# Optimization experiments

Measured on AMD Instinct MI355X. Metric: run time of the kernel, lower is better.

The kernel has to match this reference:

```python
import jax, jax.numpy as jnp
import numpy as np

D_MODEL = 1024
N_HEADS = 16
D_K = D_MODEL // N_HEADS
B, T = 4, 2048


def setup_inputs() -> dict:
    key = jax.random.key(0)
    ks = jax.random.split(key, 13)
    s = 1.0 / np.sqrt(D_MODEL)
    inp = {
        "Q": jax.random.normal(ks[0], (B, T, D_MODEL), jnp.float32),
        "K": jax.random.normal(ks[1], (B, T, D_MODEL), jnp.float32),
        "V": jax.random.normal(ks[2], (B, T, D_MODEL), jnp.float32),
        "mask": jax.random.randint(ks[3], (B, 1, 1, T), 0, 2, jnp.int32),
        "W_q": jax.random.normal(ks[4], (D_MODEL, D_MODEL), jnp.float32) * s,
        "b_q": jax.random.normal(ks[5], (D_MODEL,), jnp.float32) * s,
        "W_k": jax.random.normal(ks[6], (D_MODEL, D_MODEL), jnp.float32) * s,
        "b_k": jax.random.normal(ks[7], (D_MODEL,), jnp.float32) * s,
        "W_v": jax.random.normal(ks[8], (D_MODEL, D_MODEL), jnp.float32) * s,
        "b_v": jax.random.normal(ks[9], (D_MODEL,), jnp.float32) * s,
        "W_o": jax.random.normal(ks[10], (D_MODEL, D_MODEL), jnp.float32) * s,
        "b_o": jax.random.normal(ks[11], (D_MODEL,), jnp.float32) * s,
    }
    return inp


def _split_heads(x):
    # (B, T, d_model) -> (B, H, T, d_k)
    b, t, _ = x.shape
    return x.reshape(b, t, N_HEADS, D_K).transpose(0, 2, 1, 3)


def reference(Q, K, V, mask, W_q, b_q, W_k, b_k, W_v, b_v, W_o, b_o):
    # Linear projections (torch nn.Linear: x @ W.T + b)
    q = _split_heads(Q @ W_q.T + b_q)  # (B, H, T, d_k)
    k = _split_heads(K @ W_k.T + b_k)
    v = _split_heads(V @ W_v.T + b_v)

    scale = 1.0 / jnp.sqrt(jnp.asarray(D_K, q.dtype))
    scores = jnp.einsum('bhqd,bhkd->bhqk', q, k) * scale  # (B, H, T, T)
    scores = jnp.where(mask == 0, -jnp.inf, scores)
    attn = jax.nn.softmax(scores, axis=-1)
    out = jnp.einsum('bhqk,bhkd->bhqd', attn, v)  # (B, H, T, d_k)

    # combine heads: (B, H, T, d_k) -> (B, T, d_model)
    bsz, h, t, dk = out.shape
    out = out.transpose(0, 2, 1, 3).reshape(bsz, t, h * dk)
    return out @ W_o.T + b_o
```

## Files before the change

### kernel.cpp

```cpp
#include <hip/hip_runtime.h>
#include <hip/hip_bf16.h>
#include <stdint.h>

#define NHEADS 16
#define SEQ    2048
#define DMODEL 1024
#define DK     64

#define QB_OFF  0ull
#define KB_OFF  8388608ull
#define VB_OFF  16777216ull
#define WQ_OFF  25165824ull
#define WK_OFF  26214400ull
#define WV_OFF  27262976ull
#define WO_OFF  28311552ull
#define QH_OFF  29360128ull
#define KH_OFF  37748736ull
#define VT_OFF  46137344ull
#define MSKF_OFF 54525952ull
#define OC_OFF  0ull

typedef __attribute__((ext_vector_type(8))) __bf16 bf16x8;
typedef __attribute__((ext_vector_type(4))) float  floatx4;

__device__ __forceinline__ unsigned short f2bf(float f) {
  unsigned int u = __float_as_uint(f);
  u += 0x7fffu + ((u >> 16) & 1u);
  return (unsigned short)(u >> 16);
}

__device__ __forceinline__ void gld_lds16(const void* g, void* l) {
  __builtin_amdgcn_global_load_lds(
      (const __attribute__((address_space(1))) unsigned int*)(g),
      (__attribute__((address_space(3))) unsigned int*)(uintptr_t)(l),
      16, 0, 0);
}

struct CastArgs {
  const float* src[8];
  unsigned long long off[8];
  unsigned int n[8];
};

__global__ __launch_bounds__(256) void cast_bf16(CastArgs a, unsigned short* __restrict__ ws) {
  int ti = blockIdx.y;
  unsigned int n = a.n[ti];
  unsigned int stride = gridDim.x * blockDim.x * 4u;
  unsigned int i0 = (blockIdx.x * blockDim.x + threadIdx.x) * 4u;
  if (ti == 7) {
    const int* s = (const int*)a.src[7];
    unsigned short* d = ws + a.off[7];
    for (unsigned int i = i0; i < n; i += stride) {
      int4 v = *(const int4*)(s + i);
      ushort4 o;
      o.x = v.x ? 0x3f80u : 0u;
      o.y = v.y ? 0x3f80u : 0u;
      o.z = v.z ? 0x3f80u : 0u;
      o.w = v.w ? 0x3f80u : 0u;
      unsigned int p = (i & ~31u) | ((i & 12u) << 1) | ((i & 16u) >> 2) | (i & 3u);
      *(ushort4*)(d + p) = o;
    }
    return;
  }
  const float* s = a.src[ti];
  unsigned short* d = ws + a.off[ti];
  for (unsigned int i = i0; i < n; i += stride) {
    float4 v = *(const float4*)(s + i);
    ushort4 o;
    o.x = f2bf(v.x); o.y = f2bf(v.y); o.z = f2bf(v.z); o.w = f2bf(v.w);
    *(ushort4*)(d + i) = o;
  }
}

__device__ __forceinline__ void gemm_core_128(
    const unsigned short* __restrict__ A, const unsigned short* __restrict__ Bw,
    int m0, int n0, unsigned short* As, unsigned short* Bs, floatx4 acc[4][4])
{
  int tid = threadIdx.x;
  int lane = tid & 63, l16 = lane & 15, quad = lane >> 4;
  int wave = tid >> 6, wm = wave >> 1, wn = wave & 1;
  #pragma unroll 1
  for (int kt = 0; kt < 32; ++kt) {
    __syncthreads();
    #pragma unroll
    for (int rnd = 0; rnd < 2; ++rnd) {
      int e = tid * 8 + rnd * 2048;
      int row = e >> 5, col = e & 31;
      gld_lds16(A  + (size_t)(m0 + row) * 1024 + kt * 32 + col, As + e);
      gld_lds16(Bw + (size_t)(n0 + row) * 1024 + kt * 32 + col, Bs + e);
    }
    __syncthreads();
    bf16x8 af[4], bfr[4];
    #pragma unroll
    for (int f = 0; f < 4; ++f) {
      af[f]  = *(const bf16x8*)(As + (wm * 64 + f * 16 + l16) * 32 + quad * 8);
      bfr[f] = *(const bf16x8*)(Bs + (wn * 64 + f * 16 + l16) * 32 + quad * 8);
    }
    #pragma unroll
    for (int fm = 0; fm < 4; ++fm)
      #pragma unroll
      for (int fn = 0; fn < 4; ++fn)
        acc[fm][fn] = __builtin_amdgcn_mfma_f32_16x16x32_bf16(af[fm], bfr[fn], acc[fm][fn], 0, 0, 0);
  }
}

__global__ __launch_bounds__(256) void proj_gemm(
    const unsigned short* __restrict__ wsc, unsigned short* __restrict__ ws,
    const float* __restrict__ bq, const float* __restrict__ bk, const float* __restrict__ bv)
{
  __shared__ unsigned short smem[17408];
  unsigned short* As = smem;
  unsigned short* Bs = smem + 4096;
  int z = blockIdx.z;
  int tid = threadIdx.x, lane = tid & 63, l16 = lane & 15, quad = lane >> 4;
  int wave = tid >> 6, wm = wave >> 1, wn = wave & 1;

  if (z < 2) {
    const unsigned short* A  = wsc + (z == 0 ? QB_OFF : KB_OFF);
    const unsigned short* Bw = wsc + (z == 0 ? WQ_OFF : WK_OFF);
    const float* bias = (z == 0) ? bq : bk;
    unsigned short* dst = ws + (z == 0 ? QH_OFF : KH_OFF);
    float scale = (z == 0) ? 0.18033688011111772f : 1.0f;

    int flat = blockIdx.y * 8 + blockIdx.x;
    int xcd = flat & 7, slot = flat >> 3;
    int m_t = xcd * 8 + (slot >> 3);
    int n_t = slot & 7;
    int m0 = m_t * 128, n0 = n_t * 128;
    floatx4 acc[4][4] = {};
    gemm_core_128(A, Bw, m0, n0, As, Bs, acc);

    __syncthreads();
    #pragma unroll
    for (int fn = 0; fn < 4; ++fn) {
      int c = wn * 64 + fn * 16 + l16;
      float bvv = bias[n0 + c];
      #pragma unroll
      for (int fm = 0; fm < 4; ++fm)
        #pragma unroll
        for (int r = 0; r < 4; ++r) {
          int t = wm * 64 + fm * 16 + quad * 4 + r;
          smem[t * 136 + c] = f2bf((acc[fm][fn][r] + bvv) * scale);
        }
    }
    __syncthreads();
    #pragma unroll
    for (int it = 0; it < 8; ++it) {
      int e = it * 2048 + tid * 8;
      int t = e >> 7, c = e & 127;
      uint4 val = *(const uint4*)(smem + t * 136 + c);
      int m = m0 + t, b = m >> 11, tg = m & 2047;
      int h = (n0 + c) >> 6, d = (n0 + c) & 63;
      *(uint4*)(dst + ((size_t)(b * NHEADS + h) * SEQ + tg) * DK + d) = val;
    }
  } else {
    int flat = blockIdx.y * 8 + blockIdx.x;
    int b = flat >> 7, rem = flat & 127;
    int mt = rem >> 4, nt = rem & 15;
    int m0 = mt * 128, n0 = nt * 128;
    const unsigned short* A  = wsc + WV_OFF;
    const unsigned short* Bw = wsc + VB_OFF + (size_t)b * SEQ * DMODEL;
    unsigned short* dst = ws + VT_OFF;

    floatx4 acc[4][4] = {};
    gemm_core_128(A, Bw, m0, n0, As, Bs, acc);

    const unsigned short* pm = wsc + MSKF_OFF + (size_t)b * SEQ;
    int tpl[4];
    float mv[4];
    #pragma unroll
    for (int fn = 0; fn < 4; ++fn) {
      int t = wn * 64 + fn * 16 + l16;
      int tp = (t & ~31) | ((t & 12) << 1) | ((t & 16) >> 2) | (t & 3);
      tpl[fn] = tp;
      mv[fn] = __uint_as_float((unsigned int)pm[n0 + tp] << 16);
    }

    __syncthreads();
    #pragma unroll
    for (int fm = 0; fm < 4; ++fm) {
      int mb = m0 + wm * 64 + fm * 16 + quad * 4;
      float4 bb4 = *(const float4*)(bv + mb);
      float bbv[4] = {bb4.x, bb4.y, bb4.z, bb4.w};
      #pragma unroll
      for (int r = 0; r < 4; ++r) {
        int mrow = wm * 64 + fm * 16 + quad * 4 + r;
        #pragma unroll
        for (int fn = 0; fn < 4; ++fn)
          smem[mrow * 136 + tpl[fn]] = f2bf((acc[fm][fn][r] + bbv[r]) * mv[fn]);
      }
    }
    __syncthreads();
    #pragma unroll
    for (int it = 0; it < 8; ++it) {
      int e = it * 2048 + tid * 8;
      int mrow = e >> 7, tcol = e & 127;
      uint4 val = *(const uint4*)(smem + mrow * 136 + tcol);
      int m = m0 + mrow, h = m >> 6, d = m & 63;
      *(uint4*)(dst + ((size_t)(b * NHEADS + h) * DK + d) * SEQ + n0 + tcol) = val;
    }
  }
}

__global__ __launch_bounds__(128, 2) void attn_fused(
    const unsigned short* __restrict__ wsc, unsigned short* __restrict__ ws)
{
  __shared__ unsigned short smem[16640];
  unsigned short* Ks  = smem;
  unsigned short* Vts = smem + 8192;
  unsigned short* MskB = smem + 16384;

  int fid = blockIdx.y * gridDim.x + blockIdx.x;
  int xcd = fid & 7, slot = fid >> 3;
  int bh = xcd * 8 + (slot >> 4);
  int qt = slot & 15;
  int b = bh >> 4, h = bh & 15;
  int tid = threadIdx.x, wave = tid >> 6, lane = tid & 63, l16 = lane & 15, quad = lane >> 4;
  int wq = wave * 64;

  const unsigned short* qh = wsc + QH_OFF + (size_t)bh * SEQ * DK;
  const unsigned short* kh = wsc + KH_OFF + (size_t)bh * SEQ * DK;
  const unsigned short* vt = wsc + VT_OFF + (size_t)bh * DK * SEQ;
  const unsigned short* pm = wsc + MSKF_OFF + (size_t)b * SEQ;

  #pragma unroll
  for (int kk = 0; kk < 2; ++kk)
    #pragma unroll
    for (int rnd = 0; rnd < 4; ++rnd) {
      int e = tid * 8 + rnd * 1024;
      int row = e >> 5, col = e & 31;
      gld_lds16(qh + (size_t)(qt * 128 + row) * DK + kk * 32 + col, Ks + kk * 4096 + e);
    }
  __syncthreads();
  bf16x8 qf[4][2];
  #pragma unroll
  for (int fq = 0; fq < 4; ++fq)
    #pragma unroll
    for (int kk = 0; kk < 2; ++kk)
      qf[fq][kk] = *(const bf16x8*)(Ks + kk * 4096 + (wq + fq * 16 + l16) * 32 + quad * 8);
  __syncthreads();

  #pragma unroll
  for (int kk = 0; kk < 2; ++kk)
    #pragma unroll
    for (int rnd = 0; rnd < 4; ++rnd) {
      int e = tid * 8 + rnd * 1024;
      int row = e >> 5, col = e & 31;
      gld_lds16(kh + (size_t)row * DK + kk * 32 + col, Ks + kk * 4096 + e);
    }
  if (tid < 16)
    gld_lds16(pm + tid * 8, MskB + tid * 8);
  __syncthreads();

  floatx4 o[4][4] = {};
  floatx4 osum[4] = {};
  const floatx4 zero4 = {};

  union PU { unsigned int u[4][4]; bf16x8 v[4]; };

  #pragma unroll 1
  for (int jt = 0; jt < 16; ++jt) {
    #pragma unroll
    for (int kk = 0; kk < 4; ++kk)
      #pragma unroll
      for (int rnd = 0; rnd < 2; ++rnd) {
        int e = tid * 8 + rnd * 1024;
        int row = e >> 5, col = e & 31;
        gld_lds16(vt + (size_t)row * SEQ + jt * 128 + kk * 32 + col, Vts + kk * 2048 + e);
      }

    PU pf[4];
    #pragma unroll
    for (int w = 0; w < 4; ++w) {
      floatx4 s[2][4];
      #pragma unroll
      for (int f2 = 0; f2 < 2; ++f2) {
        int fk = 2 * w + f2;
        bf16x8 kf0 = *(const bf16x8*)(Ks +        (fk * 16 + l16) * 32 + quad * 8);
        bf16x8 kf1 = *(const bf16x8*)(Ks + 4096 + (fk * 16 + l16) * 32 + quad * 8);
        #pragma unroll
        for (int fq = 0; fq < 4; ++fq) {
          s[f2][fq] = __builtin_amdgcn_mfma_f32_16x16x32_bf16(kf0, qf[fq][0], zero4, 0, 0, 0);
          s[f2][fq] = __builtin_amdgcn_mfma_f32_16x16x32_bf16(kf1, qf[fq][1], s[f2][fq], 0, 0, 0);
        }
      }
      #pragma unroll
      for (int f2 = 0; f2 < 2; ++f2)
        #pragma unroll
        for (int fq = 0; fq < 4; ++fq)
          #pragma unroll
          for (int r = 0; r < 4; ++r)
            s[f2][fq][r] = __builtin_amdgcn_exp2f(s[f2][fq][r]);

      #pragma unroll
      for (int fq = 0; fq < 4; ++fq) {
        asm("v_cvt_pk_bf16_f32 %0, %1, %2" : "=v"(pf[w].u[fq][0]) : "v"(s[0][fq][0]), "v"(s[0][fq][1]));
        asm("v_cvt_pk_bf16_f32 %0, %1, %2" : "=v"(pf[w].u[fq][1]) : "v"(s[0][fq][2]), "v"(s[0][fq][3]));
        asm("v_cvt_pk_bf16_f32 %0, %1, %2" : "=v"(pf[w].u[fq][2]) : "v"(s[1][fq][0]), "v"(s[1][fq][1]));
        asm("v_cvt_pk_bf16_f32 %0, %1, %2" : "=v"(pf[w].u[fq][3]) : "v"(s[1][fq][2]), "v"(s[1][fq][3]));
      }

      bf16x8 mvf = *(const bf16x8*)(MskB + w * 32 + quad * 8);
      #pragma unroll
      for (int fq = 0; fq < 4; ++fq)
        osum[fq] = __builtin_amdgcn_mfma_f32_16x16x32_bf16(mvf, pf[w].v[fq], osum[fq], 0, 0, 0);
    }

    __syncthreads();

    if (jt < 15) {
      const unsigned short* khn = kh + (size_t)(jt + 1) * 128 * DK;
      #pragma unroll
      for (int kk = 0; kk < 2; ++kk)
        #pragma unroll
        for (int rnd = 0; rnd < 4; ++rnd) {
          int e = tid * 8 + rnd * 1024;
          int row = e >> 5, col = e & 31;
          gld_lds16(khn + (size_t)row * DK + kk * 32 + col, Ks + kk * 4096 + e);
        }
      if (tid < 16)
        gld_lds16(pm + (jt + 1) * 128 + tid * 8, MskB + tid * 8);
    }

    __builtin_amdgcn_s_setprio(1);
    #pragma unroll
    for (int w = 0; w < 4; ++w)
      #pragma unroll
      for (int fd = 0; fd < 4; ++fd) {
        bf16x8 vf = *(const bf16x8*)(Vts + w * 2048 + (fd * 16 + l16) * 32 + quad * 8);
        #pragma unroll
        for (int fq = 0; fq < 4; ++fq)
          o[fd][fq] = __builtin_amdgcn_mfma_f32_16x16x32_bf16(vf, pf[w].v[fq], o[fd][fq], 0, 0, 0);
      }
    __builtin_amdgcn_s_setprio(0);

    __syncthreads();
  }

  float inv[4];
  #pragma unroll
  for (int fq = 0; fq < 4; ++fq)
    inv[fq] = __builtin_amdgcn_rcpf(osum[fq][0]);

  unsigned short* Ot = smem;
  #pragma unroll
  for (int fd = 0; fd < 4; ++fd)
    #pragma unroll
    for (int fq = 0; fq < 4; ++fq)
      #pragma unroll
      for (int r = 0; r < 4; ++r) {
        int q = wq + fq * 16 + l16;
        int d = fd * 16 + quad * 4 + r;
        Ot[q * 72 + d] = f2bf(o[fd][fq][r] * inv[fq]);
      }
  __syncthreads();
  unsigned short* oc = ws + OC_OFF;
  #pragma unroll
  for (int rr = 0; rr < 8; ++rr) {
    int e = rr * 1024 + tid * 8;
    int q = e >> 6, off = e & 63;
    uint4 val = *(const uint4*)(Ot + q * 72 + off);
    *(uint4*)(oc + ((size_t)(b * SEQ + qt * 128 + q)) * DMODEL + h * DK + off) = val;
  }
}

__global__ __launch_bounds__(256) void out_gemm(
    const unsigned short* __restrict__ wsc, const float* __restrict__ bo,
    float* __restrict__ out)
{
  __shared__ unsigned short smem[8192];
  unsigned short* As = smem;
  unsigned short* Bs = smem + 4096;
  int flat = blockIdx.y * 8 + blockIdx.x;
  int xcd = flat & 7, slot = flat >> 3;
  int m_t = xcd * 8 + (slot >> 3);
  int n_t = slot & 7;
  int m0 = m_t * 128, n0 = n_t * 128;
  floatx4 acc[4][4] = {};
  gemm_core_128(wsc + OC_OFF, wsc + WO_OFF, m0, n0, As, Bs, acc);

  int tid = threadIdx.x, lane = tid & 63, l16 = lane & 15, quad = lane >> 4;
  int wave = tid >> 6, wm = wave >> 1, wn = wave & 1;
  #pragma unroll
  for (int fn = 0; fn < 4; ++fn) {
    int n = n0 + wn * 64 + fn * 16 + l16;
    float bvv = bo[n];
    #pragma unroll
    for (int fm = 0; fm < 4; ++fm)
      #pragma unroll
      for (int r = 0; r < 4; ++r) {
        int m = m0 + wm * 64 + fm * 16 + quad * 4 + r;
        out[(size_t)m * DMODEL + n] = acc[fm][fn][r] + bvv;
      }
  }
}

extern "C" void kernel_launch(void* const* d_in, const int* in_sizes, int n_in,
                              void* d_out, int out_size, void* d_ws, size_t ws_size,
                              hipStream_t stream) {
  const float* Q    = (const float*)d_in[0];
  const float* K    = (const float*)d_in[1];
  const float* V    = (const float*)d_in[2];
  const float* bq   = (const float*)d_in[5];
  const float* bk   = (const float*)d_in[7];
  const float* bv   = (const float*)d_in[9];
  const float* bo   = (const float*)d_in[11];
  unsigned short* ws = (unsigned short*)d_ws;
  float* out = (float*)d_out;

  CastArgs ca;
  ca.src[0] = Q;  ca.src[1] = K;  ca.src[2] = V;
  ca.src[3] = (const float*)d_in[4]; ca.src[4] = (const float*)d_in[6];
  ca.src[5] = (const float*)d_in[8]; ca.src[6] = (const float*)d_in[10];
  ca.src[7] = (const float*)d_in[3];
  ca.off[0] = QB_OFF; ca.off[1] = KB_OFF; ca.off[2] = VB_OFF;
  ca.off[3] = WQ_OFF; ca.off[4] = WK_OFF; ca.off[5] = WV_OFF; ca.off[6] = WO_OFF;
  ca.off[7] = MSKF_OFF;
  ca.n[0] = ca.n[1] = ca.n[2] = 8388608u;
  ca.n[3] = ca.n[4] = ca.n[5] = ca.n[6] = 1048576u;
  ca.n[7] = 8192u;

  hipLaunchKernelGGL(cast_bf16, dim3(2048, 8), dim3(256), 0, stream, ca, ws);
  hipLaunchKernelGGL(proj_gemm, dim3(8, 64, 3), dim3(256), 0, stream, ws, ws, bq, bk, bv);
  hipLaunchKernelGGL(attn_fused, dim3(16, 64), dim3(128), 0, stream, ws, ws);
  hipLaunchKernelGGL(out_gemm, dim3(8, 64), dim3(256), 0, stream, ws, bo, out);
}
```

Baseline: 334.4 us.

## Double-buffer LDS tiles in shared GEMM core and raise MFMA wave priority

The 128x128 GEMM core now keeps two LDS stages. It issues the global-to-LDS loads for k-tile kt+1 before running the MFMAs on tile kt, so copy latency overlaps compute and each k-step needs one barrier instead of two. The MFMA block is wrapped in s_setprio to favour waves that are issuing matrix work. The out-projection kernel's shared buffer doubles to fit both stages, which raises LDS use per block and may lower occupancy. Correctness relies on the barrier waiting for the outstanding direct-to-LDS loads.

Result: faster. 311.7 us (-6.8%).

```diff
diff --git a/kernel.cpp b/kernel.cpp
--- a/kernel.cpp
+++ b/kernel.cpp
@@ -74,33 +74,54 @@
 
 __device__ __forceinline__ void gemm_core_128(
     const unsigned short* __restrict__ A, const unsigned short* __restrict__ Bw,
-    int m0, int n0, unsigned short* As, unsigned short* Bs, floatx4 acc[4][4])
+    int m0, int n0, unsigned short* sm, floatx4 acc[4][4])
 {
   int tid = threadIdx.x;
   int lane = tid & 63, l16 = lane & 15, quad = lane >> 4;
   int wave = tid >> 6, wm = wave >> 1, wn = wave & 1;
+
+  #pragma unroll
+  for (int rnd = 0; rnd < 2; ++rnd) {
+    int e = tid * 8 + rnd * 2048;
+    int row = e >> 5, col = e & 31;
+    gld_lds16(A  + (size_t)(m0 + row) * 1024 + col, sm + e);
+    gld_lds16(Bw + (size_t)(n0 + row) * 1024 + col, sm + 4096 + e);
+  }
+  __syncthreads();
+
+  int cur = 0;
   #pragma unroll 1
   for (int kt = 0; kt < 32; ++kt) {
-    __syncthreads();
-    #pragma unroll
-    for (int rnd = 0; rnd < 2; ++rnd) {
-      int e = tid * 8 + rnd * 2048;
-      int row = e >> 5, col = e & 31;
-      gld_lds16(A  + (size_t)(m0 + row) * 1024 + kt * 32 + col, As + e);
-      gld_lds16(Bw + (size_t)(n0 + row) * 1024 + kt * 32 + col, Bs + e);
-    }
-    __syncthreads();
+    const unsigned short* As = sm + cur * 8192;
+    const unsigned short* Bs = As + 4096;
+
+    if (kt < 31) {
+      unsigned short* An = sm + (cur ^ 1) * 8192;
+      #pragma unroll
+      for (int rnd = 0; rnd < 2; ++rnd) {
+        int e = tid * 8 + rnd * 2048;
+        int row = e >> 5, col = e & 31;
+        gld_lds16(A  + (size_t)(m0 + row) * 1024 + (kt + 1) * 32 + col, An + e);
+        gld_lds16(Bw + (size_t)(n0 + row) * 1024 + (kt + 1) * 32 + col, An + 4096 + e);
+      }
+    }
+
     bf16x8 af[4], bfr[4];
     #pragma unroll
     for (int f = 0; f < 4; ++f) {
       af[f]  = *(const bf16x8*)(As + (wm * 64 + f * 16 + l16) * 32 + quad * 8);
       bfr[f] = *(const bf16x8*)(Bs + (wn * 64 + f * 16 + l16) * 32 + quad * 8);
     }
+    __builtin_amdgcn_s_setprio(1);
     #pragma unroll
     for (int fm = 0; fm < 4; ++fm)
       #pragma unroll
       for (int fn = 0; fn < 4; ++fn)
         acc[fm][fn] = __builtin_amdgcn_mfma_f32_16x16x32_bf16(af[fm], bfr[fn], acc[fm][fn], 0, 0, 0);
+    __builtin_amdgcn_s_setprio(0);
+
+    __syncthreads();
+    cur ^= 1;
   }
 }
 
@@ -109,8 +130,6 @@
     const float* __restrict__ bq, const float* __restrict__ bk, const float* __restrict__ bv)
 {
   __shared__ unsigned short smem[17408];
-  unsigned short* As = smem;
-  unsigned short* Bs = smem + 4096;
   int z = blockIdx.z;
   int tid = threadIdx.x, lane = tid & 63, l16 = lane & 15, quad = lane >> 4;
   int wave = tid >> 6, wm = wave >> 1, wn = wave & 1;
@@ -128,7 +147,7 @@
     int n_t = slot & 7;
     int m0 = m_t * 128, n0 = n_t * 128;
     floatx4 acc[4][4] = {};
-    gemm_core_128(A, Bw, m0, n0, As, Bs, acc);
+    gemm_core_128(A, Bw, m0, n0, smem, acc);
 
     __syncthreads();
     #pragma unroll
@@ -163,7 +182,7 @@
     unsigned short* dst = ws + VT_OFF;
 
     floatx4 acc[4][4] = {};
-    gemm_core_128(A, Bw, m0, n0, As, Bs, acc);
+    gemm_core_128(A, Bw, m0, n0, smem, acc);
 
     const unsigned short* pm = wsc + MSKF_OFF + (size_t)b * SEQ;
     int tpl[4];
@@ -368,16 +387,14 @@
     const unsigned short* __restrict__ wsc, const float* __restrict__ bo,
     float* __restrict__ out)
 {
-  __shared__ unsigned short smem[8192];
-  unsigned short* As = smem;
-  unsigned short* Bs = smem + 4096;
+  __shared__ unsigned short smem[16384];
   int flat = blockIdx.y * 8 + blockIdx.x;
   int xcd = flat & 7, slot = flat >> 3;
   int m_t = xcd * 8 + (slot >> 3);
   int n_t = slot & 7;
   int m0 = m_t * 128, n0 = n_t * 128;
   floatx4 acc[4][4] = {};
-  gemm_core_128(wsc + OC_OFF, wsc + WO_OFF, m0, n0, As, Bs, acc);
+  gemm_core_128(wsc + OC_OFF, wsc + WO_OFF, m0, n0, smem, acc);
 
   int tid = threadIdx.x, lane = tid & 63, l16 = lane & 15, quad = lane >> 4;
   int wave = tid >> 6, wm = wave >> 1, wn = wave & 1;
```
